# Optimization experiments

Measured on AMD Instinct MI355X. Metric: run time of the kernel, lower is better.

The kernel has to match this reference:

```python
import jax, jax.numpy as jnp
import numpy as np

N_NODES = 50000
N_EDGES = 1000000
IN_DIM, HID_DIM, OUT_DIM = 128, 64, 16


def setup_inputs() -> dict:
    key = jax.random.key(0)
    k1, k2, k3, k4 = jax.random.split(key, 4)
    x = jax.random.normal(k1, (N_NODES, IN_DIM), dtype=jnp.float32)
    edge_index = jax.random.randint(k2, (2, N_EDGES), 0, N_NODES, dtype=jnp.int64)
    # Glorot-style scaling for weights, zero bias (PyG GCNConv default init style)
    W1 = jax.random.normal(k3, (IN_DIM, HID_DIM), dtype=jnp.float32) * (1.0 / np.sqrt(IN_DIM))
    b1 = jnp.zeros((HID_DIM,), dtype=jnp.float32)
    W2 = jax.random.normal(k4, (HID_DIM, OUT_DIM), dtype=jnp.float32) * (1.0 / np.sqrt(HID_DIM))
    b2 = jnp.zeros((OUT_DIM,), dtype=jnp.float32)
    return {"x": x, "edge_index": edge_index, "W1": W1, "b1": b1, "W2": W2, "b2": b2}


def gcn_conv(x, src, dst, W, b, num_nodes):
    """PyG GCNConv: add self loops, symmetric deg^{-1/2} normalization,
    linear transform, gather-scale-scatter aggregation, bias."""
    # degree includes self loops (src/dst already augmented by caller)
    deg = jax.ops.segment_sum(jnp.ones_like(dst, dtype=x.dtype), dst, num_segments=num_nodes)
    dinv = jnp.where(deg > 0, deg ** -0.5, 0.0)
    norm = dinv[src] * dinv[dst]            # [E']
    h = x @ W                                # [N, F_out] transform before aggregation
    msg = h[src] * norm[:, None]             # gather + scale
    out = jax.ops.segment_sum(msg, dst, num_segments=num_nodes)  # scatter-add
    return out + b


def reference(x, edge_index, W1, b1, W2, b2):
    n = x.shape[0]
    loops = jnp.arange(n, dtype=edge_index.dtype)
    src = jnp.concatenate([edge_index[0], loops])
    dst = jnp.concatenate([edge_index[1], loops])
    h = gcn_conv(x, src, dst, W1, b1, n)
    h = jax.nn.relu(h)
    out = gcn_conv(h, src, dst, W2, b2, n)
    return out
```

## Files before the change

kernel.cpp:

```cpp
#include <hip/hip_runtime.h>
#include <hip/hip_bf16.h>

#define IN_DIM 128
#define HID_DIM 64
#define OUT_DIM 16

#define SSHIFT 7
#define SMASK 127
#define CHUNK 16384
#define CBLK 1024

static __device__ __forceinline__ unsigned short f2bf(float f) {
    unsigned u = __float_as_uint(f);
    unsigned r = u + 0x7fffu + ((u >> 16) & 1u);
    return (unsigned short)(r >> 16);
}
static __device__ __forceinline__ unsigned packbf2(float a, float b) {
    return (unsigned)f2bf(a) | ((unsigned)f2bf(b) << 16);
}
static __device__ __forceinline__ float bflo(unsigned v) { return __uint_as_float(v << 16); }
static __device__ __forceinline__ float bfhi(unsigned v) { return __uint_as_float(v & 0xffff0000u); }

__global__ __launch_bounds__(CBLK) void passA(const int* __restrict__ dst,
                                              int* __restrict__ cm,
                                              int E, int NS, int NSP) {
    __shared__ int cnt[512];
    int t = threadIdx.x;
    for (int s = t; s < NS; s += CBLK) cnt[s] = 0;
    __syncthreads();
    int base = blockIdx.x * CHUNK;
    #pragma unroll 4
    for (int k = 0; k < CHUNK; k += CBLK) {
        int i = base + k + t;
        if (i < E) atomicAdd(&cnt[dst[i] >> SSHIFT], 1);
    }
    __syncthreads();
    for (int s = t; s < NS; s += CBLK) cm[blockIdx.x * NSP + s] = cnt[s];
}

__global__ __launch_bounds__(64) void passB1(int* __restrict__ cm, int* __restrict__ tot,
                                             int B, int NSP) {
    __shared__ int sv[64];
    int t = threadIdx.x, s = blockIdx.x;
    int v = (t < B) ? cm[t * NSP + s] : 0;
    sv[t] = v;
    __syncthreads();
    for (int off = 1; off < 64; off <<= 1) {
        int tmp = (t >= off) ? sv[t - off] : 0;
        __syncthreads();
        sv[t] += tmp;
        __syncthreads();
    }
    if (t < B) cm[t * NSP + s] = sv[t] - v;
    if (t == 63) tot[s] = sv[63];
}

__global__ __launch_bounds__(512) void passB2(const int* __restrict__ tot,
                                              int* __restrict__ sbase, int NS) {
    __shared__ int sv[512];
    int t = threadIdx.x;
    int v = (t < NS) ? tot[t] : 0;
    sv[t] = v;
    __syncthreads();
    for (int off = 1; off < 512; off <<= 1) {
        int tmp = (t >= off) ? sv[t - off] : 0;
        __syncthreads();
        sv[t] += tmp;
        __syncthreads();
    }
    if (t < NS) sbase[t] = sv[t] - v;
}

__global__ __launch_bounds__(CBLK) void passC(const int* __restrict__ src,
                                              const int* __restrict__ dst,
                                              const int* __restrict__ cm,
                                              const int* __restrict__ sbase,
                                              int* __restrict__ eb,
                                              int E, int NS, int NSP) {
    __shared__ int cur[512];
    int t = threadIdx.x, b = blockIdx.x;
    for (int s = t; s < NS; s += CBLK) cur[s] = sbase[s] + cm[b * NSP + s];
    __syncthreads();
    int base = b * CHUNK;
    #pragma unroll 4
    for (int k = 0; k < CHUNK; k += CBLK) {
        int i = base + k + t;
        if (i < E) {
            int d = dst[i];
            int s = d >> SSHIFT;
            int pos = atomicAdd(&cur[s], 1);
            eb[pos] = src[i] | ((d & SMASK) << 17);
        }
    }
}

__global__ __launch_bounds__(256) void passD(const int* __restrict__ eb,
                                             const int* __restrict__ sbase,
                                             const int* __restrict__ tot,
                                             int* __restrict__ csr_src,
                                             int* __restrict__ row_ptr,
                                             float* __restrict__ dinv,
                                             int N, int E, int NS) {
    __shared__ int deg[128], incl[128], cur[128];
    int s = blockIdx.x, t = threadIdx.x;
    if (t < 128) deg[t] = 0;
    __syncthreads();
    int b0 = sbase[s], cnt = tot[s];
    for (int k = t; k < cnt; k += 256) atomicAdd(&deg[eb[b0 + k] >> 17], 1);
    __syncthreads();
    if (t < 128) incl[t] = deg[t];
    __syncthreads();
    for (int off = 1; off < 128; off <<= 1) {
        int tmp = 0;
        if (t < 128 && t >= off) tmp = incl[t - off];
        __syncthreads();
        if (t < 128) incl[t] += tmp;
        __syncthreads();
    }
    if (t < 128) {
        int loff = incl[t] - deg[t];
        cur[t] = b0 + loff;
        int n = (s << SSHIFT) + t;
        if (n < N) {
            row_ptr[n] = b0 + loff;
            dinv[n] = rsqrtf((float)(deg[t] + 1));
        }
    }
    if (s == NS - 1 && t == 0) row_ptr[N] = E;
    __syncthreads();
    for (int k = t; k < cnt; k += 256) {
        int v = eb[b0 + k];
        int dl = v >> 17;
        int p = atomicAdd(&cur[dl], 1);
        csr_src[p] = v & 0x1FFFF;
    }
}

__global__ __launch_bounds__(256) void gemm1_kernel(const float* __restrict__ x,
                                                    const float* __restrict__ W1,
                                                    const float* __restrict__ dinv,
                                                    unsigned* __restrict__ h1u, int N) {
    __shared__ __align__(16) float sW[IN_DIM * HID_DIM];
    __shared__ __align__(16) float sx[16 * IN_DIM];
    int t = threadIdx.x;
    int node0 = blockIdx.x * 16;

    const float4* W4  = (const float4*)W1;
    float4*       sW4 = (float4*)sW;
    for (int i = t; i < (IN_DIM * HID_DIM) / 4; i += 256) sW4[i] = W4[i];

    const float4* x4  = (const float4*)x;
    float4*       sx4 = (float4*)sx;
    for (int i = t; i < (16 * IN_DIM) / 4; i += 256) {
        int r = i >> 5, c = i & 31;
        int n = node0 + r; if (n >= N) n = 0;
        sx4[(r << 5) + c] = x4[(size_t)n * 32 + c];
    }
    __syncthreads();

    int ln = t >> 4, jj = t & 15;
    int n = node0 + ln;
    float4 acc = {0.f, 0.f, 0.f, 0.f};
    const float* xr = sx + ln * IN_DIM;
    #pragma unroll 4
    for (int k = 0; k < IN_DIM; ++k) {
        float  xk = xr[k];
        float4 wv = ((const float4*)(sW + k * HID_DIM))[jj];
        acc.x += xk * wv.x; acc.y += xk * wv.y; acc.z += xk * wv.z; acc.w += xk * wv.w;
    }
    if (n <= N) {
        float dn = (n < N) ? dinv[n] : 0.f;
        uint2 pv;
        pv.x = packbf2(acc.x * dn, acc.y * dn);
        pv.y = packbf2(acc.z * dn, acc.w * dn);
        ((uint2*)(h1u + (size_t)n * 32))[jj] = pv;
    }
}

__global__ __launch_bounds__(256) void agg1_kernel(const unsigned* __restrict__ h1u,
                                                   const int* __restrict__ row_ptr,
                                                   const int* __restrict__ csr_src,
                                                   const float* __restrict__ dinv,
                                                   const float* __restrict__ b1,
                                                   unsigned* __restrict__ h1au, int N) {
    int t = threadIdx.x;
    int n = blockIdx.x * 4 + (t >> 6);
    if (n >= N) return;
    int lane = t & 63;
    int half = lane >> 5;
    int l    = lane & 31;

    int srow = half ? N : n;
    unsigned v = h1u[(size_t)srow * 32 + l];
    float ax = bflo(v), ay = bfhi(v);

    int e1 = row_ptr[n + 1];
    int e  = row_ptr[n];
    for (; e + 8 <= e1; e += 8) {
        int s0 = csr_src[e + 0 + half];
        int s1 = csr_src[e + 2 + half];
        int s2 = csr_src[e + 4 + half];
        int s3 = csr_src[e + 6 + half];
        unsigned v0 = h1u[(size_t)s0 * 32 + l];
        unsigned v1 = h1u[(size_t)s1 * 32 + l];
        unsigned v2 = h1u[(size_t)s2 * 32 + l];
        unsigned v3 = h1u[(size_t)s3 * 32 + l];
        ax += bflo(v0) + bflo(v1) + bflo(v2) + bflo(v3);
        ay += bfhi(v0) + bfhi(v1) + bfhi(v2) + bfhi(v3);
    }
    for (; e < e1; e += 2) {
        int idx = e + half;
        int s = (idx < e1) ? csr_src[idx] : N;
        unsigned vv = h1u[(size_t)s * 32 + l];
        ax += bflo(vv);
        ay += bfhi(vv);
    }
    ax += __shfl_xor(ax, 32);
    ay += __shfl_xor(ay, 32);
    if (half == 0) {
        float dn = dinv[n];
        float2 bb = ((const float2*)b1)[l];
        float r0 = fmaxf(fmaf(dn, ax, bb.x), 0.f);
        float r1 = fmaxf(fmaf(dn, ay, bb.y), 0.f);
        h1au[(size_t)n * 32 + l] = packbf2(r0, r1);
    }
}

__global__ __launch_bounds__(256) void gemm2_kernel(const unsigned* __restrict__ h1au,
                                                    const float* __restrict__ W2,
                                                    const float* __restrict__ dinv,
                                                    unsigned* __restrict__ h2u, int N) {
    __shared__ __align__(16) float sW[HID_DIM * OUT_DIM];
    __shared__ __align__(16) float sx[16 * HID_DIM];
    int t = threadIdx.x;
    int node0 = blockIdx.x * 16;

    ((float4*)sW)[t] = ((const float4*)W2)[t];
    for (int i = t; i < 512; i += 256) {
        int r = i >> 5, c = i & 31;
        int n = node0 + r; if (n >= N) n = 0;
        unsigned v = h1au[(size_t)n * 32 + c];
        float2 f; f.x = bflo(v); f.y = bfhi(v);
        *(float2*)(sx + r * HID_DIM + 2 * c) = f;
    }
    __syncthreads();

    int ln = t >> 4, j = t & 15;
    float acc = 0.f;
    const float* xr = sx + ln * HID_DIM;
    #pragma unroll 8
    for (int k = 0; k < HID_DIM; ++k) acc += xr[k] * sW[k * OUT_DIM + j];
    int n = node0 + ln;
    float other = __shfl_xor(acc, 1);
    if (n <= N && (j & 1) == 0) {
        float dn = (n < N) ? dinv[n] : 0.f;
        h2u[(size_t)n * 8 + (j >> 1)] = packbf2(acc * dn, other * dn);
    }
}

__global__ __launch_bounds__(256) void agg2_kernel(const unsigned* __restrict__ h2u,
                                                   const int* __restrict__ row_ptr,
                                                   const int* __restrict__ csr_src,
                                                   const float* __restrict__ dinv,
                                                   const float* __restrict__ b2,
                                                   float* __restrict__ out, int N) {
    int t = threadIdx.x;
    int n = blockIdx.x * 16 + (t >> 4);
    if (n >= N) return;
    int half = (t >> 3) & 1;
    int l    = t & 7;

    int srow = half ? N : n;
    unsigned v = h2u[(size_t)srow * 8 + l];
    float ax = bflo(v), ay = bfhi(v);

    int e1 = row_ptr[n + 1];
    int e  = row_ptr[n];
    for (; e + 8 <= e1; e += 8) {
        int s0 = csr_src[e + 0 + half];
        int s1 = csr_src[e + 2 + half];
        int s2 = csr_src[e + 4 + half];
        int s3 = csr_src[e + 6 + half];
        unsigned v0 = h2u[(size_t)s0 * 8 + l];
        unsigned v1 = h2u[(size_t)s1 * 8 + l];
        unsigned v2 = h2u[(size_t)s2 * 8 + l];
        unsigned v3 = h2u[(size_t)s3 * 8 + l];
        ax += bflo(v0) + bflo(v1) + bflo(v2) + bflo(v3);
        ay += bfhi(v0) + bfhi(v1) + bfhi(v2) + bfhi(v3);
    }
    for (; e < e1; e += 2) {
        int idx = e + half;
        int s = (idx < e1) ? csr_src[idx] : N;
        unsigned vv = h2u[(size_t)s * 8 + l];
        ax += bflo(vv);
        ay += bfhi(vv);
    }
    ax += __shfl_xor(ax, 8);
    ay += __shfl_xor(ay, 8);
    if (half == 0) {
        float dn = dinv[n];
        float2 bb = ((const float2*)b2)[l];
        float2 r;
        r.x = fmaf(dn, ax, bb.x);
        r.y = fmaf(dn, ay, bb.y);
        ((float2*)out)[(size_t)n * 8 + l] = r;
    }
}

extern "C" void kernel_launch(void* const* d_in, const int* in_sizes, int n_in,
                              void* d_out, int out_size, void* d_ws, size_t ws_size,
                              hipStream_t stream) {
    const float* x  = (const float*)d_in[0];
    const int*   ei = (const int*)d_in[1];
    const float* W1 = (const float*)d_in[2];
    const float* b1 = (const float*)d_in[3];
    const float* W2 = (const float*)d_in[4];
    const float* b2 = (const float*)d_in[5];
    float* out = (float*)d_out;

    const int N = in_sizes[0] / IN_DIM;
    const int E = in_sizes[1] / 2;
    const int* src = ei;
    const int* dst = ei + E;

    const int NS  = (N + SMASK) >> SSHIFT;
    const int NSP = NS + 1;
    const int BC  = (E + CHUNK - 1) / CHUNK;

    char* w = (char*)d_ws;
    auto alloc = [&](size_t bytes) -> void* {
        void* p = (void*)w;
        w += (bytes + 255) & ~(size_t)255;
        return p;
    };
    int*      cm      = (int*)     alloc((size_t)BC * NSP * 4);
    int*      tot     = (int*)     alloc((size_t)NS * 4);
    int*      sbase   = (int*)     alloc((size_t)NS * 4);
    int*      eb      = (int*)     alloc((size_t)E * 4);
    int*      csr_src = (int*)     alloc((size_t)E * 4);
    int*      row_ptr = (int*)     alloc((size_t)(N + 1) * 4);
    float*    dinv    = (float*)   alloc((size_t)N * 4);
    unsigned* h1u     = (unsigned*)alloc((size_t)(N + 1) * 32 * 4);
    unsigned* h1au    = (unsigned*)alloc((size_t)(N + 1) * 32 * 4);
    unsigned* h2u     = (unsigned*)alloc((size_t)(N + 1) * 8 * 4);

    const int GB = (N + 16) / 16;

    passA <<<BC, CBLK, 0, stream>>>(dst, cm, E, NS, NSP);
    passB1<<<NS, 64,   0, stream>>>(cm, tot, BC, NSP);
    passB2<<<1,  512,  0, stream>>>(tot, sbase, NS);
    passC <<<BC, CBLK, 0, stream>>>(src, dst, cm, sbase, eb, E, NS, NSP);
    passD <<<NS, 256,  0, stream>>>(eb, sbase, tot, csr_src, row_ptr, dinv, N, E, NS);

    gemm1_kernel<<<GB, 256, 0, stream>>>(x, W1, dinv, h1u, N);
    agg1_kernel<<<(N + 3) / 4, 256, 0, stream>>>(h1u, row_ptr, csr_src, dinv, b1, h1au, N);
    gemm2_kernel<<<GB, 256, 0, stream>>>(h1au, W2, dinv, h2u, N);
    agg2_kernel<<<GB, 256, 0, stream>>>(h2u, row_ptr, csr_src, dinv, b2, out, N);
}
```

Baseline: 190.2 us.

## Vectorize aggregation gathers with cooperative index loads and shuffled broadcast

Both aggregation kernels now load up to 64 neighbor indices per wave in a single coalesced read and broadcast them with shuffles. Each lane then gathers 16-byte (agg1) or 8-byte (agg2) chunks of a row, so 8 or 16 edges are handled per wave step instead of 2. agg2 goes from 16 threads per node to a full wave per node, followed by a cross-lane reduction. This is meant to cut redundant index loads and raise memory-level parallelism, at the cost of idle lanes on low-degree nodes and extra shuffle-reduction work.

```diff
diff --git a/kernel.cpp b/kernel.cpp
--- a/kernel.cpp
+++ b/kernel.cpp
@@ -187,42 +187,61 @@
     int n = blockIdx.x * 4 + (t >> 6);
     if (n >= N) return;
     int lane = t & 63;
-    int half = lane >> 5;
-    int l    = lane & 31;
-
-    int srow = half ? N : n;
-    unsigned v = h1u[(size_t)srow * 32 + l];
-    float ax = bflo(v), ay = bfhi(v);
-
-    int e1 = row_ptr[n + 1];
-    int e  = row_ptr[n];
-    for (; e + 8 <= e1; e += 8) {
-        int s0 = csr_src[e + 0 + half];
-        int s1 = csr_src[e + 2 + half];
-        int s2 = csr_src[e + 4 + half];
-        int s3 = csr_src[e + 6 + half];
-        unsigned v0 = h1u[(size_t)s0 * 32 + l];
-        unsigned v1 = h1u[(size_t)s1 * 32 + l];
-        unsigned v2 = h1u[(size_t)s2 * 32 + l];
-        unsigned v3 = h1u[(size_t)s3 * 32 + l];
-        ax += bflo(v0) + bflo(v1) + bflo(v2) + bflo(v3);
-        ay += bfhi(v0) + bfhi(v1) + bfhi(v2) + bfhi(v3);
-    }
-    for (; e < e1; e += 2) {
-        int idx = e + half;
-        int s = (idx < e1) ? csr_src[idx] : N;
-        unsigned vv = h1u[(size_t)s * 32 + l];
-        ax += bflo(vv);
-        ay += bfhi(vv);
-    }
-    ax += __shfl_xor(ax, 32);
-    ay += __shfl_xor(ay, 32);
-    if (half == 0) {
+    int es = lane >> 3;
+    int dg = lane & 7;
+
+    int e0 = row_ptr[n], e1 = row_ptr[n + 1];
+    const uint4* rb = (const uint4*)h1u;
+
+    float a0 = 0.f, a1 = 0.f, a2 = 0.f, a3 = 0.f,
+          a4 = 0.f, a5 = 0.f, a6 = 0.f, a7 = 0.f;
+
+    for (int base = e0 - 1; base < e1; base += 64) {
+        int idx = base + lane;
+        int sld = N;
+        if (idx == e0 - 1) sld = n;
+        else if (idx < e1) sld = csr_src[idx];
+        int lim = e1 - base;
+        int nr = (lim + 7) >> 3;
+        nr = (nr + 1) & ~1;
+        for (int r = 0; r < nr; r += 2) {
+            int sA = __shfl(sld, (r << 3) + es);
+            int sB = __shfl(sld, ((r + 1) << 3) + es);
+            uint4 vA = rb[(size_t)sA * 8 + dg];
+            uint4 vB = rb[(size_t)sB * 8 + dg];
+            a0 += bflo(vA.x) + bflo(vB.x);
+            a1 += bfhi(vA.x) + bfhi(vB.x);
+            a2 += bflo(vA.y) + bflo(vB.y);
+            a3 += bfhi(vA.y) + bfhi(vB.y);
+            a4 += bflo(vA.z) + bflo(vB.z);
+            a5 += bfhi(vA.z) + bfhi(vB.z);
+            a6 += bflo(vA.w) + bflo(vB.w);
+            a7 += bfhi(vA.w) + bfhi(vB.w);
+        }
+    }
+    #pragma unroll
+    for (int m = 8; m <= 32; m <<= 1) {
+        a0 += __shfl_xor(a0, m); a1 += __shfl_xor(a1, m);
+        a2 += __shfl_xor(a2, m); a3 += __shfl_xor(a3, m);
+        a4 += __shfl_xor(a4, m); a5 += __shfl_xor(a5, m);
+        a6 += __shfl_xor(a6, m); a7 += __shfl_xor(a7, m);
+    }
+    if (es == 0) {
         float dn = dinv[n];
-        float2 bb = ((const float2*)b1)[l];
-        float r0 = fmaxf(fmaf(dn, ax, bb.x), 0.f);
-        float r1 = fmaxf(fmaf(dn, ay, bb.y), 0.f);
-        h1au[(size_t)n * 32 + l] = packbf2(r0, r1);
+        float4 bA = ((const float4*)b1)[2 * dg];
+        float4 bB = ((const float4*)b1)[2 * dg + 1];
+        float r0 = fmaxf(fmaf(dn, a0, bA.x), 0.f);
+        float r1 = fmaxf(fmaf(dn, a1, bA.y), 0.f);
+        float r2 = fmaxf(fmaf(dn, a2, bA.z), 0.f);
+        float r3 = fmaxf(fmaf(dn, a3, bA.w), 0.f);
+        float r4 = fmaxf(fmaf(dn, a4, bB.x), 0.f);
+        float r5 = fmaxf(fmaf(dn, a5, bB.y), 0.f);
+        float r6 = fmaxf(fmaf(dn, a6, bB.z), 0.f);
+        float r7 = fmaxf(fmaf(dn, a7, bB.w), 0.f);
+        uint4 pv;
+        pv.x = packbf2(r0, r1); pv.y = packbf2(r2, r3);
+        pv.z = packbf2(r4, r5); pv.w = packbf2(r6, r7);
+        ((uint4*)h1au)[(size_t)n * 8 + dg] = pv;
     }
 }
 
@@ -265,45 +284,50 @@
                                                    const float* __restrict__ b2,
                                                    float* __restrict__ out, int N) {
     int t = threadIdx.x;
-    int n = blockIdx.x * 16 + (t >> 4);
+    int n = blockIdx.x * 4 + (t >> 6);
     if (n >= N) return;
-    int half = (t >> 3) & 1;
-    int l    = t & 7;
-
-    int srow = half ? N : n;
-    unsigned v = h2u[(size_t)srow * 8 + l];
-    float ax = bflo(v), ay = bfhi(v);
-
-    int e1 = row_ptr[n + 1];
-    int e  = row_ptr[n];
-    for (; e + 8 <= e1; e += 8) {
-        int s0 = csr_src[e + 0 + half];
-        int s1 = csr_src[e + 2 + half];
-        int s2 = csr_src[e + 4 + half];
-        int s3 = csr_src[e + 6 + half];
-        unsigned v0 = h2u[(size_t)s0 * 8 + l];
-        unsigned v1 = h2u[(size_t)s1 * 8 + l];
-        unsigned v2 = h2u[(size_t)s2 * 8 + l];
-        unsigned v3 = h2u[(size_t)s3 * 8 + l];
-        ax += bflo(v0) + bflo(v1) + bflo(v2) + bflo(v3);
-        ay += bfhi(v0) + bfhi(v1) + bfhi(v2) + bfhi(v3);
-    }
-    for (; e < e1; e += 2) {
-        int idx = e + half;
-        int s = (idx < e1) ? csr_src[idx] : N;
-        unsigned vv = h2u[(size_t)s * 8 + l];
-        ax += bflo(vv);
-        ay += bfhi(vv);
-    }
-    ax += __shfl_xor(ax, 8);
-    ay += __shfl_xor(ay, 8);
-    if (half == 0) {
+    int lane = t & 63;
+    int es = lane >> 2;
+    int dg = lane & 3;
+
+    int e0 = row_ptr[n], e1 = row_ptr[n + 1];
+    const uint2* rb = (const uint2*)h2u;
+
+    float a0 = 0.f, a1 = 0.f, a2 = 0.f, a3 = 0.f;
+
+    for (int base = e0 - 1; base < e1; base += 64) {
+        int idx = base + lane;
+        int sld = N;
+        if (idx == e0 - 1) sld = n;
+        else if (idx < e1) sld = csr_src[idx];
+        int lim = e1 - base;
+        int nr = (lim + 15) >> 4;
+        nr = (nr + 1) & ~1;
+        for (int r = 0; r < nr; r += 2) {
+            int sA = __shfl(sld, (r << 4) + es);
+            int sB = __shfl(sld, ((r + 1) << 4) + es);
+            uint2 vA = rb[(size_t)sA * 4 + dg];
+            uint2 vB = rb[(size_t)sB * 4 + dg];
+            a0 += bflo(vA.x) + bflo(vB.x);
+            a1 += bfhi(vA.x) + bfhi(vB.x);
+            a2 += bflo(vA.y) + bflo(vB.y);
+            a3 += bfhi(vA.y) + bfhi(vB.y);
+        }
+    }
+    #pragma unroll
+    for (int m = 4; m <= 32; m <<= 1) {
+        a0 += __shfl_xor(a0, m); a1 += __shfl_xor(a1, m);
+        a2 += __shfl_xor(a2, m); a3 += __shfl_xor(a3, m);
+    }
+    if (es == 0) {
         float dn = dinv[n];
-        float2 bb = ((const float2*)b2)[l];
-        float2 r;
-        r.x = fmaf(dn, ax, bb.x);
-        r.y = fmaf(dn, ay, bb.y);
-        ((float2*)out)[(size_t)n * 8 + l] = r;
+        float4 bb = ((const float4*)b2)[dg];
+        float4 r;
+        r.x = fmaf(dn, a0, bb.x);
+        r.y = fmaf(dn, a1, bb.y);
+        r.z = fmaf(dn, a2, bb.z);
+        r.w = fmaf(dn, a3, bb.w);
+        ((float4*)out)[(size_t)n * 4 + dg] = r;
     }
 }
 
@@ -345,6 +369,7 @@
     unsigned* h2u     = (unsigned*)alloc((size_t)(N + 1) * 8 * 4);
 
     const int GB = (N + 16) / 16;
+    const int AB = (N + 3) / 4;
 
     passA <<<BC, CBLK, 0, stream>>>(dst, cm, E, NS, NSP);
     passB1<<<NS, 64,   0, stream>>>(cm, tot, BC, NSP);
@@ -353,7 +378,7 @@
     passD <<<NS, 256,  0, stream>>>(eb, sbase, tot, csr_src, row_ptr, dinv, N, E, NS);
 
     gemm1_kernel<<<GB, 256, 0, stream>>>(x, W1, dinv, h1u, N);
-    agg1_kernel<<<(N + 3) / 4, 256, 0, stream>>>(h1u, row_ptr, csr_src, dinv, b1, h1au, N);
+    agg1_kernel<<<AB, 256, 0, stream>>>(h1u, row_ptr, csr_src, dinv, b1, h1au, N);
     gemm2_kernel<<<GB, 256, 0, stream>>>(h1au, W2, dinv, h2u, N);
-    agg2_kernel<<<GB, 256, 0, stream>>>(h2u, row_ptr, csr_src, dinv, b2, out, N);
-}
+    agg2_kernel<<<AB, 256, 0, stream>>>(h2u, row_ptr, csr_src, dinv, b2, out, N);
+}
```

New measurement: 187.4 us. Within noise of the previous version (-1.4%).
